# Optimization experiments

Hardware: AMD Instinct MI355X
Metric: run time of the kernel (lower is better)

## Reference

```python
import jax, jax.numpy as jnp
import numpy as np

HEADS = 8
DIM_HEAD = 64
LN_EPS = 1e-5


def _layernorm(x, gamma, beta):
    mu = jnp.mean(x, axis=-1, keepdims=True)
    var = jnp.var(x, axis=-1, keepdims=True)
    return (x - mu) * jax.lax.rsqrt(var + LN_EPS) * gamma + beta


def setup_inputs() -> dict:
    key = jax.random.key(0)
    ks = jax.random.split(key, 5)
    B, N, D = 1, 16384, 512
    return {
        "x": jax.random.normal(ks[0], (B, N, D), dtype=jnp.float32),
        "ln_gamma": jnp.ones((D,), dtype=jnp.float32),
        "ln_beta": jnp.zeros((D,), dtype=jnp.float32),
        "w_qkv": jax.random.normal(ks[1], (D, 3 * D), dtype=jnp.float32) * (D ** -0.5),
        "agent": jax.random.normal(ks[2], (HEADS, 512, DIM_HEAD), dtype=jnp.float32) * (DIM_HEAD ** -0.5),
        "w_out": jax.random.normal(ks[3], (D, D), dtype=jnp.float32) * (D ** -0.5),
        "b_out": jnp.zeros((D,), dtype=jnp.float32),
    }


def reference(x, ln_gamma, ln_beta, w_qkv, agent, w_out, b_out):
    # TransLayer: x + Mask_Agent_Attention(LayerNorm(x))
    B, N, D = x.shape
    xn = _layernorm(x, ln_gamma, ln_beta)

    qkv = xn @ w_qkv                                   # [B, N, 3D]
    q, k, v = jnp.split(qkv, 3, axis=-1)
    # [B, H, N, d]
    q = q.reshape(B, N, HEADS, DIM_HEAD).transpose(0, 2, 1, 3)
    k = k.reshape(B, N, HEADS, DIM_HEAD).transpose(0, 2, 1, 3)
    v = v.reshape(B, N, HEADS, DIM_HEAD).transpose(0, 2, 1, 3)

    scale = DIM_HEAD ** -0.5  # tem=0 -> classical 1/sqrt(d) scaling

    # agents aggregate values: softmax over keys  [B, H, A, N]
    attn1 = jax.nn.softmax(jnp.einsum('had,bhnd->bhan', agent, k) * scale, axis=-1)
    agent_v = jnp.einsum('bhan,bhnd->bhad', attn1, v)  # [B, H, A, d]

    # queries attend to agents: softmax over agents  [B, H, N, A]
    attn2 = jax.nn.softmax(jnp.einsum('bhnd,had->bhna', q, agent) * scale, axis=-1)
    out = jnp.einsum('bhna,bhad->bhnd', attn2, agent_v)  # [B, H, N, d]

    out = out + v  # residual=True: value residual inside attention
    out = out.transpose(0, 2, 1, 3).reshape(B, N, D)
    out = out @ w_out + b_out
    return x + out
```

## Files before the change

### kernel.cpp

```cpp
#include <hip/hip_runtime.h>
#include <stdint.h>

typedef unsigned short u16;
typedef __attribute__((ext_vector_type(8))) short bf16x8;
typedef __attribute__((ext_vector_type(4))) float f32x4;

__device__ __forceinline__ float bf2f(u16 u){
  union { uint32_t i; float f; } v; v.i = ((uint32_t)u) << 16; return v.f;
}
__device__ __forceinline__ u16 f2bf(float f){
  union { float fl; uint32_t i; } v; v.fl = f;
  uint32_t r = v.i + 0x7FFFu + ((v.i >> 16) & 1u);
  return (u16)(r >> 16);
}
__device__ __forceinline__ uint32_t cvt_pk_bf16(float lo, float hi){
  uint32_t r;
  asm("v_cvt_pk_bf16_f32 %0, %1, %2" : "=v"(r) : "v"(lo), "v"(hi));
  return r;
}
__device__ __forceinline__ f32x4 mfma16(bf16x8 a, bf16x8 b, f32x4 c){
  return __builtin_amdgcn_mfma_f32_16x16x32_bf16(a, b, c, 0, 0, 0);
}
__device__ __forceinline__ void gload16(const u16* g, u16* l){
  __builtin_amdgcn_global_load_lds((const __attribute__((address_space(1))) void*)g,
                                   (__attribute__((address_space(3))) void*)l, 16, 0, 0);
}

__global__ __launch_bounds__(256) void k_conv_bf(const float* __restrict__ in, u16* __restrict__ out, int n, float scale){
  int i = (blockIdx.x * 256 + threadIdx.x) * 4;
  if (i >= n) return;
  float4 v = *(const float4*)(in + i);
  ushort4 o; o.x=f2bf(v.x*scale); o.y=f2bf(v.y*scale); o.z=f2bf(v.z*scale); o.w=f2bf(v.w*scale);
  *(ushort4*)(out + i) = o;
}

__global__ __launch_bounds__(256) void k_transp(const float* __restrict__ in, u16* __restrict__ out, int R, int C){
  __shared__ u16 tile[64][68];
  int c0 = blockIdx.x * 64, r0 = blockIdx.y * 64;
  int tr = threadIdx.x >> 4;
  int tc = (threadIdx.x & 15) * 4;
  for (int rr = 0; rr < 4; rr++){
    int r = rr * 16 + tr;
    float4 v = *(const float4*)(in + (size_t)(r0 + r) * C + c0 + tc);
    ushort4 o; o.x=f2bf(v.x); o.y=f2bf(v.y); o.z=f2bf(v.z); o.w=f2bf(v.w);
    *(ushort4*)&tile[r][tc] = o;
  }
  __syncthreads();
  for (int rr = 0; rr < 4; rr++){
    int oc = rr * 16 + tr;
    ushort4 o;
    o.x = tile[tc+0][oc]; o.y = tile[tc+1][oc]; o.z = tile[tc+2][oc]; o.w = tile[tc+3][oc];
    *(ushort4*)(out + (size_t)(c0 + oc) * R + r0 + tc) = o;
  }
}

__global__ __launch_bounds__(256) void k_transp_v(const u16* __restrict__ qkv, u16* __restrict__ vT){
  __shared__ u16 tile[64][68];
  int n0 = blockIdx.x * 64;
  int c0 = blockIdx.y * 64;
  int tr = threadIdx.x >> 4;
  int tc = (threadIdx.x & 15) * 4;
  for (int rr = 0; rr < 4; rr++){
    int r = rr * 16 + tr;
    ushort4 v = *(const ushort4*)(qkv + (size_t)(n0 + r) * 1536 + 1024 + c0 + tc);
    *(ushort4*)&tile[r][tc] = v;
  }
  __syncthreads();
  for (int rr = 0; rr < 4; rr++){
    int oc = rr * 16 + tr;
    ushort4 o;
    o.x = tile[tc+0][oc]; o.y = tile[tc+1][oc]; o.z = tile[tc+2][oc]; o.w = tile[tc+3][oc];
    *(ushort4*)(vT + (size_t)(c0 + oc) * 16384 + n0 + tc) = o;
  }
}

__global__ __launch_bounds__(128) void k_ln(const float* __restrict__ x, const float* __restrict__ g,
                                            const float* __restrict__ b, u16* __restrict__ xn){
  int row = blockIdx.x;
  int t = threadIdx.x;
  float4 v = *(const float4*)(x + (size_t)row * 512 + t * 4);
  float s = v.x + v.y + v.z + v.w;
  float q = v.x*v.x + v.y*v.y + v.z*v.z + v.w*v.w;
  for (int o = 32; o > 0; o >>= 1){ s += __shfl_down(s, o); q += __shfl_down(q, o); }
  __shared__ float red[4];
  if ((t & 63) == 0){ red[(t >> 6) * 2] = s; red[(t >> 6) * 2 + 1] = q; }
  __syncthreads();
  float mu  = (red[0] + red[2]) * (1.0f/512.0f);
  float var = (red[1] + red[3]) * (1.0f/512.0f) - mu * mu;
  float rs = rsqrtf(var + 1e-5f);
  float4 gv = *(const float4*)(g + t * 4);
  float4 bv = *(const float4*)(b + t * 4);
  ushort4 o;
  o.x = f2bf((v.x - mu) * rs * gv.x + bv.x);
  o.y = f2bf((v.y - mu) * rs * gv.y + bv.y);
  o.z = f2bf((v.z - mu) * rs * gv.z + bv.z);
  o.w = f2bf((v.w - mu) * rs * gv.w + bv.w);
  *(ushort4*)(xn + (size_t)row * 512 + t * 4) = o;
}


__global__ __launch_bounds__(512) void k_gemm_qkv(const u16* __restrict__ A, const u16* __restrict__ Bt,
                                                  u16* __restrict__ C){
  __shared__ u16 aL[2][256 * 64];
  __shared__ u16 bL[2][128 * 64];
  int m0 = blockIdx.x * 256, n0 = blockIdx.y * 128;
  int t = threadIdx.x, w = t >> 6, l = t & 63;
  int wm = (w >> 1) * 64, wn = (w & 1) * 64;
  int lr = l & 15;
  int blkSrc = (l & 7) ^ ((l >> 3) & 7);
  const u16* gA = A  + (size_t)(m0 + w*8 + (l >> 3)) * 512 + blkSrc * 8;
  const u16* gB = Bt + (size_t)(n0 + w*8 + (l >> 3)) * 512 + blkSrc * 8;
  f32x4 acc[4][4];
  for (int i=0;i<4;i++) for (int j=0;j<4;j++) acc[i][j] = {0.f,0.f,0.f,0.f};

  auto stage = [&](int buf, int k0){
    #pragma unroll
    for (int p = 0; p < 4; p++)
      gload16(gA + (size_t)p*64*512 + k0, &aL[buf][(p*64 + w*8) * 64]);
    #pragma unroll
    for (int p = 0; p < 2; p++)
      gload16(gB + (size_t)p*64*512 + k0, &bL[buf][(p*64 + w*8) * 64]);
  };
  auto comp = [&](const u16* ab, const u16* bb){
    #pragma unroll
    for (int kk = 0; kk < 64; kk += 32){
      int xo = (((l >> 4) + (kk >> 3)) ^ (l & 7)) << 3;
      bf16x8 av[4], bv[4];
      #pragma unroll
      for (int mt=0;mt<4;mt++) av[mt] = *(const bf16x8*)&ab[(wm + mt*16 + lr)*64 + xo];
      #pragma unroll
      for (int nt=0;nt<4;nt++) bv[nt] = *(const bf16x8*)&bb[(wn + nt*16 + lr)*64 + xo];
      #pragma unroll
      for (int mt=0;mt<4;mt++)
        #pragma unroll
        for (int nt=0;nt<4;nt++)
          acc[mt][nt] = mfma16(av[mt], bv[nt], acc[mt][nt]);
    }
  };

  stage(0, 0);
  __syncthreads();
  #pragma unroll
  for (int tk = 0; tk < 8; tk++){
    int cur = tk & 1;
    if (tk < 7) stage(cur ^ 1, (tk + 1) * 64);
    comp(&aL[cur][0], &bL[cur][0]);
    __syncthreads();
  }

  int rr = (l >> 4) * 4, cc = l & 15;
  for (int mt=0;mt<4;mt++) for (int nt=0;nt<4;nt++)
    for (int j=0;j<4;j++){
      int r = m0 + wm + mt*16 + rr + j;
      int c = n0 + wn + nt*16 + cc;
      C[(size_t)r * 1536 + c] = f2bf(acc[mt][nt][j]);
    }
}

__global__ __launch_bounds__(512) void k_gemm_out(const u16* __restrict__ A, const u16* __restrict__ Bt,
                                                  const float* __restrict__ x, const float* __restrict__ bias,
                                                  float* __restrict__ y){
  __shared__ u16 aL[2][256 * 64];
  __shared__ u16 bL[2][128 * 64];
  int m0 = blockIdx.x * 256, n0 = blockIdx.y * 128;
  int t = threadIdx.x, w = t >> 6, l = t & 63;
  int wm = (w >> 1) * 64, wn = (w & 1) * 64;
  int lr = l & 15;
  int blkSrc = (l & 7) ^ ((l >> 3) & 7);
  const u16* gA = A  + (size_t)(m0 + w*8 + (l >> 3)) * 512 + blkSrc * 8;
  const u16* gB = Bt + (size_t)(n0 + w*8 + (l >> 3)) * 512 + blkSrc * 8;
  f32x4 acc[4][4];
  for (int i=0;i<4;i++) for (int j=0;j<4;j++) acc[i][j] = {0.f,0.f,0.f,0.f};

  auto stage = [&](int buf, int k0){
    #pragma unroll
    for (int p = 0; p < 4; p++)
      gload16(gA + (size_t)p*64*512 + k0, &aL[buf][(p*64 + w*8) * 64]);
    #pragma unroll
    for (int p = 0; p < 2; p++)
      gload16(gB + (size_t)p*64*512 + k0, &bL[buf][(p*64 + w*8) * 64]);
  };
  auto comp = [&](const u16* ab, const u16* bb){
    #pragma unroll
    for (int kk = 0; kk < 64; kk += 32){
      int xo = (((l >> 4) + (kk >> 3)) ^ (l & 7)) << 3;
      bf16x8 av[4], bv[4];
      #pragma unroll
      for (int mt=0;mt<4;mt++) av[mt] = *(const bf16x8*)&ab[(wm + mt*16 + lr)*64 + xo];
      #pragma unroll
      for (int nt=0;nt<4;nt++) bv[nt] = *(const bf16x8*)&bb[(wn + nt*16 + lr)*64 + xo];
      #pragma unroll
      for (int mt=0;mt<4;mt++)
        #pragma unroll
        for (int nt=0;nt<4;nt++)
          acc[mt][nt] = mfma16(av[mt], bv[nt], acc[mt][nt]);
    }
  };

  stage(0, 0);
  __syncthreads();
  #pragma unroll
  for (int tk = 0; tk < 8; tk++){
    int cur = tk & 1;
    if (tk < 7) stage(cur ^ 1, (tk + 1) * 64);
    comp(&aL[cur][0], &bL[cur][0]);
    __syncthreads();
  }

  int rr = (l >> 4) * 4, cc = l & 15;
  for (int mt=0;mt<4;mt++) for (int nt=0;nt<4;nt++)
    for (int j=0;j<4;j++){
      int r = m0 + wm + mt*16 + rr + j;
      int c = n0 + wn + nt*16 + cc;
      y[(size_t)r * 512 + c] = acc[mt][nt][j] + bias[c] + x[(size_t)r * 512 + c];
    }
}

__global__ __launch_bounds__(256) void k_agent_agg(const u16* __restrict__ agbf, const u16* __restrict__ qkv,
                                                   const u16* __restrict__ vT,
                                                   float* __restrict__ nump, float* __restrict__ denp){
  int L = blockIdx.x;
  int g = (L >> 6) * 8 + (L & 7);
  int m = (L >> 3) & 7;
  int h = g >> 4, ch = g & 15, a0 = m * 64;

  __shared__ u16 ag[64][72];
  __shared__ u16 kt[64][72];
  __shared__ u16 vt[64][72];
  __shared__ u16 pt[64][72];
  int t = threadIdx.x, w = t >> 6, l = t & 63;

  for (int i = 0; i < 2; i++){
    int flat = t + 256 * i;
    int r = flat >> 3, c = (flat & 7) * 8;
    *(uint4*)&ag[r][c] = *(const uint4*)(agbf + (size_t)(h * 512 + a0 + r) * 64 + c);
  }

  bf16x8 ones;
  for (int i = 0; i < 8; i++) ones[i] = (short)0x3F80;

  f32x4 acc2[4];
  for (int i=0;i<4;i++) acc2[i] = {0.f,0.f,0.f,0.f};
  f32x4 accd = {0.f,0.f,0.f,0.f};

  for (int sub = 0; sub < 16; sub++){
    int n0 = ch * 1024 + sub * 64;
    __syncthreads();
    {
      int flat = t;
      int r = flat >> 3, c = (flat & 7) * 8;
      *(uint4*)&kt[r][c] = *(const uint4*)(qkv + (size_t)(n0 + r) * 1536 + 512 + h * 64 + c);
      int flat2 = t + 256;
      int r2 = flat2 >> 3, c2 = (flat2 & 7) * 8;
      *(uint4*)&kt[r2][c2] = *(const uint4*)(qkv + (size_t)(n0 + r2) * 1536 + 512 + h * 64 + c2);
      *(uint4*)&vt[r][c]   = *(const uint4*)(vT + ((size_t)(h * 64 + r) << 14) + n0 + c);
      *(uint4*)&vt[r2][c2] = *(const uint4*)(vT + ((size_t)(h * 64 + r2) << 14) + n0 + c2);
    }
    __syncthreads();

    f32x4 s[4];
    for (int nt=0;nt<4;nt++) s[nt] = {0.f,0.f,0.f,0.f};
    for (int kk = 0; kk < 64; kk += 32){
      int kb = kk + (l >> 4) * 8;
      bf16x8 kf = *(const bf16x8*)&kt[w*16 + (l & 15)][kb];
      for (int nt=0;nt<4;nt++){
        bf16x8 af = *(const bf16x8*)&ag[nt*16 + (l & 15)][kb];
        s[nt] = mfma16(kf, af, s[nt]);
      }
    }
    int nb = w*16 + (l >> 4) * 4;
    for (int nt=0;nt<4;nt++){
      int a = nt*16 + (l & 15);
      uint32_t w0 = cvt_pk_bf16(__builtin_amdgcn_exp2f(s[nt][0]), __builtin_amdgcn_exp2f(s[nt][1]));
      uint32_t w1 = cvt_pk_bf16(__builtin_amdgcn_exp2f(s[nt][2]), __builtin_amdgcn_exp2f(s[nt][3]));
      uint2 o; o.x = w0; o.y = w1;
      *(uint2*)&pt[a][nb] = o;
    }
    __syncthreads();

    for (int kk = 0; kk < 64; kk += 32){
      int kb = kk + (l >> 4) * 8;
      bf16x8 vf = *(const bf16x8*)&vt[w*16 + (l & 15)][kb];
      for (int mt=0;mt<4;mt++){
        bf16x8 pf = *(const bf16x8*)&pt[mt*16 + (l & 15)][kb];
        acc2[mt] = mfma16(pf, vf, acc2[mt]);
      }
      bf16x8 pw = *(const bf16x8*)&pt[w*16 + (l & 15)][kb];
      accd = mfma16(ones, pw, accd);
    }
  }

  size_t base = ((size_t)(h * 16 + ch) * 512 + a0) * 64;
  for (int mt=0;mt<4;mt++)
    #pragma unroll
    for (int j=0;j<4;j++){
      int a = mt*16 + (l>>4)*4 + j;
      int d = w*16 + (l&15);
      nump[base + (size_t)a*64 + d] = acc2[mt][j];
    }
  if (l < 16) denp[(size_t)(h*16 + ch) * 512 + a0 + w*16 + l] = accd[0];
}

__global__ __launch_bounds__(64) void k_agent_reduce(const float* __restrict__ nump, const float* __restrict__ denp,
                                                     u16* __restrict__ avtg){
  int h = blockIdx.x >> 9;
  int a = blockIdx.x & 511;
  int d = threadIdx.x;
  float num = 0.f, den = 0.f;
  for (int c = 0; c < 16; c++){
    num += nump[((size_t)(h * 16 + c) * 512 + a) * 64 + d];
    den += denp[(size_t)(h * 16 + c) * 512 + a];
  }
  avtg[((size_t)h * 64 + d) * 512 + a] = f2bf(num / den);
}

__global__ __launch_bounds__(256) void k_qattn(const u16* __restrict__ qkv, const u16* __restrict__ agbf,
                                               const u16* __restrict__ avtg, u16* __restrict__ atto){
  int n0 = blockIdx.x * 64;
  int h  = blockIdx.y;
  __shared__ u16 qt[64][72];
  __shared__ u16 ag[64][72];
  __shared__ u16 avt[64][72];
  __shared__ u16 pt[64][72];
  __shared__ float dnf[64];
  int t = threadIdx.x, w = t >> 6, l = t & 63;

  for (int i = 0; i < 2; i++){
    int flat = t + 256 * i;
    int r = flat >> 3, c = (flat & 7) * 8;
    *(uint4*)&qt[r][c] = *(const uint4*)(qkv + (size_t)(n0 + r) * 1536 + h * 64 + c);
  }

  bf16x8 ones;
  for (int i = 0; i < 8; i++) ones[i] = (short)0x3F80;

  f32x4 acc[4];
  for (int i=0;i<4;i++) acc[i] = {0.f,0.f,0.f,0.f};
  f32x4 accd = {0.f,0.f,0.f,0.f};

  for (int at = 0; at < 8; at++){
    int a0 = at * 64;
    __syncthreads();
    for (int i = 0; i < 2; i++){
      int flat = t + 256 * i;
      int r = flat >> 3, c = (flat & 7) * 8;
      *(uint4*)&ag[r][c]  = *(const uint4*)(agbf + (size_t)(h * 512 + a0 + r) * 64 + c);
      *(uint4*)&avt[r][c] = *(const uint4*)(avtg + (size_t)(h * 64 + r) * 512 + a0 + c);
    }
    __syncthreads();

    f32x4 s[4];
    for (int nt=0;nt<4;nt++) s[nt] = {0.f,0.f,0.f,0.f};
    for (int kk = 0; kk < 64; kk += 32){
      int kb = kk + (l >> 4) * 8;
      bf16x8 af = *(const bf16x8*)&ag[w*16 + (l & 15)][kb];
      for (int nt=0;nt<4;nt++){
        bf16x8 qf = *(const bf16x8*)&qt[nt*16 + (l & 15)][kb];
        s[nt] = mfma16(af, qf, s[nt]);
      }
    }
    int ab = w*16 + (l >> 4) * 4;
    for (int nt=0;nt<4;nt++){
      int n = nt*16 + (l & 15);
      uint32_t w0 = cvt_pk_bf16(__builtin_amdgcn_exp2f(s[nt][0]), __builtin_amdgcn_exp2f(s[nt][1]));
      uint32_t w1 = cvt_pk_bf16(__builtin_amdgcn_exp2f(s[nt][2]), __builtin_amdgcn_exp2f(s[nt][3]));
      uint2 o; o.x = w0; o.y = w1;
      *(uint2*)&pt[n][ab] = o;
    }
    __syncthreads();

    for (int kk = 0; kk < 64; kk += 32){
      int kb = kk + (l >> 4) * 8;
      bf16x8 vf = *(const bf16x8*)&avt[w*16 + (l & 15)][kb];
      for (int mt=0;mt<4;mt++){
        bf16x8 pf = *(const bf16x8*)&pt[mt*16 + (l & 15)][kb];
        acc[mt] = mfma16(pf, vf, acc[mt]);
      }
      bf16x8 pw = *(const bf16x8*)&pt[w*16 + (l & 15)][kb];
      accd = mfma16(ones, pw, accd);
    }
  }

  if (l < 16) dnf[w*16 + l] = accd[0];
  __syncthreads();
  if (t < 64) dnf[t] = __builtin_amdgcn_rcpf(dnf[t]);
  __syncthreads();

  int d = w*16 + (l & 15);
  for (int mt=0;mt<4;mt++){
    #pragma unroll
    for (int j=0;j<4;j++){
      int n = mt*16 + (l>>4)*4 + j;
      float v = bf2f(qkv[(size_t)(n0 + n) * 1536 + 1024 + h * 64 + d]);
      atto[(size_t)(n0 + n) * 512 + h * 64 + d] = f2bf(acc[mt][j] * dnf[n] + v);
    }
  }
}

extern "C" void kernel_launch(void* const* d_in, const int* in_sizes, int n_in,
                              void* d_out, int out_size, void* d_ws, size_t ws_size,
                              hipStream_t stream) {
  const float* x     = (const float*)d_in[0];
  const float* gamma = (const float*)d_in[1];
  const float* beta  = (const float*)d_in[2];
  const float* w_qkv = (const float*)d_in[3];
  const float* agent = (const float*)d_in[4];
  const float* w_out = (const float*)d_in[5];
  const float* b_out = (const float*)d_in[6];
  float* y = (float*)d_out;

  char* ws = (char*)d_ws;
  u16*   xn    = (u16*)  (ws + 0);
  u16*   vT    = (u16*)  (ws + 0);
  u16*   qkv   = (u16*)  (ws + 16777216);
  u16*   wqkvt = (u16*)  (ws + 67108864);
  u16*   woutt = (u16*)  (ws + 68681728);
  u16*   agbf  = (u16*)  (ws + 69206016);
  u16*   avtg  = (u16*)  (ws + 69730304);
  u16*   atto  = (u16*)  (ws + 70254592);
  float* nump  = (float*)(ws + 87031808);
  float* denp  = (float*)(ws + 103809024);

  k_conv_bf   <<<dim3(256),     dim3(256), 0, stream>>>(agent, agbf, 8*512*64, 0.125f * 1.44269504089f);
  k_transp    <<<dim3(24, 8),   dim3(256), 0, stream>>>(w_qkv, wqkvt, 512, 1536);
  k_transp    <<<dim3(8, 8),    dim3(256), 0, stream>>>(w_out, woutt, 512, 512);
  k_ln        <<<dim3(16384),   dim3(128), 0, stream>>>(x, gamma, beta, xn);
  k_gemm_qkv  <<<dim3(64, 12),  dim3(512), 0, stream>>>(xn, wqkvt, qkv);
  k_transp_v  <<<dim3(256, 8),  dim3(256), 0, stream>>>(qkv, vT);
  k_agent_agg <<<dim3(1024),    dim3(256), 0, stream>>>(agbf, qkv, vT, nump, denp);
  k_agent_reduce<<<dim3(4096),  dim3(64),  0, stream>>>(nump, denp, avtg);
  k_qattn     <<<dim3(256, 8),  dim3(256), 0, stream>>>(qkv, agbf, avtg, atto);
  k_gemm_out  <<<dim3(64, 4),   dim3(512), 0, stream>>>(atto, woutt, x, b_out, y);
}
```

Baseline: 167.6 us.

## Restructure query-attention kernel with register P, agent-split warps and register prefetch

The query-to-agent attention kernel now keeps Q fragments and the exp-score tile in registers and feeds P straight into the second MFMA, with no LDS round trip for P. Each warp handles a different slice of agents for all 64 rows and d columns, processes 128 agents per step, and prefetches the next agent/agent-V tile into registers. The per-warp partial outputs and denominators are reduced across warps through LDS at the end, and the residual add and bf16 store are vectorized. This removes per-tile syncs and P shared-memory traffic, at the cost of more accumulator registers (64 floats) and an LDS cross-warp reduction.

```diff
diff --git a/kernel.cpp b/kernel.cpp
--- a/kernel.cpp
+++ b/kernel.cpp
@@ -318,81 +318,156 @@
                                                const u16* __restrict__ avtg, u16* __restrict__ atto){
   int n0 = blockIdx.x * 64;
   int h  = blockIdx.y;
-  __shared__ u16 qt[64][72];
-  __shared__ u16 ag[64][72];
-  __shared__ u16 avt[64][72];
-  __shared__ u16 pt[64][72];
-  __shared__ float dnf[64];
+  __shared__ char sm[35840];
+  __shared__ float dnf[4][64];
+  u16 (*agL)[72]  = (u16(*)[72])sm;
+  u16 (*avL)[136] = (u16(*)[136])(sm + 18432);
+  float* red0 = (float*)sm;
+  float* red1 = red0 + 64*68;
+
   int t = threadIdx.x, w = t >> 6, l = t & 63;
-
-  for (int i = 0; i < 2; i++){
-    int flat = t + 256 * i;
-    int r = flat >> 3, c = (flat & 7) * 8;
-    *(uint4*)&qt[r][c] = *(const uint4*)(qkv + (size_t)(n0 + r) * 1536 + h * 64 + c);
-  }
-
-  bf16x8 ones;
-  for (int i = 0; i < 8; i++) ones[i] = (short)0x3F80;
-
-  f32x4 acc[4];
-  for (int i=0;i<4;i++) acc[i] = {0.f,0.f,0.f,0.f};
-  f32x4 accd = {0.f,0.f,0.f,0.f};
-
-  for (int at = 0; at < 8; at++){
-    int a0 = at * 64;
-    __syncthreads();
-    for (int i = 0; i < 2; i++){
-      int flat = t + 256 * i;
-      int r = flat >> 3, c = (flat & 7) * 8;
-      *(uint4*)&ag[r][c]  = *(const uint4*)(agbf + (size_t)(h * 512 + a0 + r) * 64 + c);
-      *(uint4*)&avt[r][c] = *(const uint4*)(avtg + (size_t)(h * 64 + r) * 512 + a0 + c);
-    }
-    __syncthreads();
-
-    f32x4 s[4];
-    for (int nt=0;nt<4;nt++) s[nt] = {0.f,0.f,0.f,0.f};
-    for (int kk = 0; kk < 64; kk += 32){
-      int kb = kk + (l >> 4) * 8;
-      bf16x8 af = *(const bf16x8*)&ag[w*16 + (l & 15)][kb];
+  int lr = l & 15, q4 = l >> 4;
+
+  bf16x8 qf[4][2];
+  #pragma unroll
+  for (int nt=0;nt<4;nt++)
+    #pragma unroll
+    for (int kk=0;kk<2;kk++)
+      qf[nt][kk] = *(const bf16x8*)(qkv + (size_t)(n0 + nt*16 + lr) * 1536 + h*64 + kk*32 + q4*8);
+
+  uint4 sAg[4], sAv[4];
+  #pragma unroll
+  for (int i=0;i<4;i++){
+    int c = t + 256*i;
+    sAg[i] = *(const uint4*)(agbf + (size_t)(h*512 + (c>>3)) * 64 + (c&7)*8);
+    sAv[i] = *(const uint4*)(avtg + (size_t)(h*64 + (c>>4)) * 512 + (c&15)*8);
+  }
+
+  f32x4 acc[4][4];
+  #pragma unroll
+  for (int i=0;i<4;i++)
+    #pragma unroll
+    for (int j=0;j<4;j++) acc[i][j] = {0.f,0.f,0.f,0.f};
+  float den[4] = {0.f,0.f,0.f,0.f};
+
+  for (int p = 0; p < 4; p++){
+    __syncthreads();
+    #pragma unroll
+    for (int i=0;i<4;i++){
+      int c = t + 256*i;
+      *(uint4*)&agL[c>>3][(c&7)*8]  = sAg[i];
+      *(uint4*)&avL[c>>4][(c&15)*8] = sAv[i];
+    }
+    __syncthreads();
+    if (p < 3){
+      #pragma unroll
+      for (int i=0;i<4;i++){
+        int c = t + 256*i;
+        sAg[i] = *(const uint4*)(agbf + (size_t)(h*512 + (p+1)*128 + (c>>3)) * 64 + (c&7)*8);
+        sAv[i] = *(const uint4*)(avtg + (size_t)(h*64 + (c>>4)) * 512 + (p+1)*128 + (c&15)*8);
+      }
+    }
+
+    uint32_t pk[2][4][2];
+    #pragma unroll
+    for (int t2 = 0; t2 < 2; t2++){
+      f32x4 s[4];
+      #pragma unroll
+      for (int nt=0;nt<4;nt++) s[nt] = {0.f,0.f,0.f,0.f};
+      #pragma unroll
+      for (int kk=0;kk<2;kk++){
+        bf16x8 af = *(const bf16x8*)&agL[t2*64 + w*16 + lr][q4*8 + kk*32];
+        #pragma unroll
+        for (int nt=0;nt<4;nt++)
+          s[nt] = mfma16(af, qf[nt][kk], s[nt]);
+      }
+      #pragma unroll
       for (int nt=0;nt<4;nt++){
-        bf16x8 qf = *(const bf16x8*)&qt[nt*16 + (l & 15)][kb];
-        s[nt] = mfma16(af, qf, s[nt]);
+        float e0 = __builtin_amdgcn_exp2f(s[nt][0]);
+        float e1 = __builtin_amdgcn_exp2f(s[nt][1]);
+        float e2 = __builtin_amdgcn_exp2f(s[nt][2]);
+        float e3 = __builtin_amdgcn_exp2f(s[nt][3]);
+        den[nt] += (e0 + e1) + (e2 + e3);
+        pk[t2][nt][0] = cvt_pk_bf16(e0, e1);
+        pk[t2][nt][1] = cvt_pk_bf16(e2, e3);
       }
     }
-    int ab = w*16 + (l >> 4) * 4;
-    for (int nt=0;nt<4;nt++){
-      int n = nt*16 + (l & 15);
-      uint32_t w0 = cvt_pk_bf16(__builtin_amdgcn_exp2f(s[nt][0]), __builtin_amdgcn_exp2f(s[nt][1]));
-      uint32_t w1 = cvt_pk_bf16(__builtin_amdgcn_exp2f(s[nt][2]), __builtin_amdgcn_exp2f(s[nt][3]));
-      uint2 o; o.x = w0; o.y = w1;
-      *(uint2*)&pt[n][ab] = o;
-    }
-    __syncthreads();
-
-    for (int kk = 0; kk < 64; kk += 32){
-      int kb = kk + (l >> 4) * 8;
-      bf16x8 vf = *(const bf16x8*)&avt[w*16 + (l & 15)][kb];
-      for (int mt=0;mt<4;mt++){
-        bf16x8 pf = *(const bf16x8*)&pt[mt*16 + (l & 15)][kb];
-        acc[mt] = mfma16(pf, vf, acc[mt]);
+    #pragma unroll
+    for (int dt=0;dt<4;dt++){
+      uint2 b0 = *(const uint2*)&avL[dt*16 + lr][w*16 + q4*4];
+      uint2 b1 = *(const uint2*)&avL[dt*16 + lr][64 + w*16 + q4*4];
+      union { uint32_t u[4]; bf16x8 v; } bb;
+      bb.u[0] = b0.x; bb.u[1] = b0.y; bb.u[2] = b1.x; bb.u[3] = b1.y;
+      #pragma unroll
+      for (int nt=0;nt<4;nt++){
+        union { uint32_t u[4]; bf16x8 v; } aa;
+        aa.u[0] = pk[0][nt][0]; aa.u[1] = pk[0][nt][1];
+        aa.u[2] = pk[1][nt][0]; aa.u[3] = pk[1][nt][1];
+        acc[nt][dt] = mfma16(aa.v, bb.v, acc[nt][dt]);
       }
-      bf16x8 pw = *(const bf16x8*)&pt[w*16 + (l & 15)][kb];
-      accd = mfma16(ones, pw, accd);
-    }
-  }
-
-  if (l < 16) dnf[w*16 + l] = accd[0];
-  __syncthreads();
-  if (t < 64) dnf[t] = __builtin_amdgcn_rcpf(dnf[t]);
-  __syncthreads();
-
-  int d = w*16 + (l & 15);
-  for (int mt=0;mt<4;mt++){
-    #pragma unroll
-    for (int j=0;j<4;j++){
-      int n = mt*16 + (l>>4)*4 + j;
-      float v = bf2f(qkv[(size_t)(n0 + n) * 1536 + 1024 + h * 64 + d]);
-      atto[(size_t)(n0 + n) * 512 + h * 64 + d] = f2bf(acc[mt][j] * dnf[n] + v);
+    }
+  }
+
+  float dq[4];
+  #pragma unroll
+  for (int nt=0;nt<4;nt++){
+    float r = den[nt];
+    r += __shfl_xor(r, 16);
+    r += __shfl_xor(r, 32);
+    dq[nt] = r;
+  }
+  __syncthreads();
+  if (q4 == 0)
+    #pragma unroll
+    for (int nt=0;nt<4;nt++) dnf[w][nt*16 + lr] = dq[nt];
+  if (w < 2){
+    float* r = (w == 0) ? red0 : red1;
+    #pragma unroll
+    for (int nt=0;nt<4;nt++)
+      #pragma unroll
+      for (int dt=0;dt<4;dt++)
+        #pragma unroll
+        for (int j=0;j<4;j++)
+          r[(nt*16 + q4*4 + j)*68 + dt*16 + lr] = acc[nt][dt][j];
+  }
+  __syncthreads();
+  if (w >= 2){
+    float* r = (w == 2) ? red0 : red1;
+    #pragma unroll
+    for (int nt=0;nt<4;nt++)
+      #pragma unroll
+      for (int dt=0;dt<4;dt++)
+        #pragma unroll
+        for (int j=0;j<4;j++)
+          r[(nt*16 + q4*4 + j)*68 + dt*16 + lr] += acc[nt][dt][j];
+  }
+  __syncthreads();
+
+  {
+    int n = t & 63, db = t >> 6;
+    float dsum = dnf[0][n] + dnf[1][n] + dnf[2][n] + dnf[3][n];
+    float rc = __builtin_amdgcn_rcpf(dsum);
+    const u16* vres = qkv + (size_t)(n0 + n) * 1536 + 1024 + h*64 + db*16;
+    u16* op = atto + (size_t)(n0 + n) * 512 + h*64 + db*16;
+    #pragma unroll
+    for (int half = 0; half < 2; half++){
+      f32x4 ra = *(f32x4*)&red0[n*68 + db*16 + half*8];
+      f32x4 rb = *(f32x4*)&red0[n*68 + db*16 + half*8 + 4];
+      f32x4 sa = *(f32x4*)&red1[n*68 + db*16 + half*8];
+      f32x4 sb = *(f32x4*)&red1[n*68 + db*16 + half*8 + 4];
+      ushort4 v0 = *(const ushort4*)(vres + half*8);
+      ushort4 v1 = *(const ushort4*)(vres + half*8 + 4);
+      ushort4 o0, o1;
+      o0.x = f2bf((ra[0]+sa[0])*rc + bf2f(v0.x));
+      o0.y = f2bf((ra[1]+sa[1])*rc + bf2f(v0.y));
+      o0.z = f2bf((ra[2]+sa[2])*rc + bf2f(v0.z));
+      o0.w = f2bf((ra[3]+sa[3])*rc + bf2f(v0.w));
+      o1.x = f2bf((rb[0]+sb[0])*rc + bf2f(v1.x));
+      o1.y = f2bf((rb[1]+sb[1])*rc + bf2f(v1.y));
+      o1.z = f2bf((rb[2]+sb[2])*rc + bf2f(v1.z));
+      o1.w = f2bf((rb[3]+sb[3])*rc + bf2f(v1.w));
+      *(ushort4*)(op + half*8) = o0;
+      *(ushort4*)(op + half*8 + 4) = o1;
     }
   }
 }
```

Result: slower. 211.9 us (+26.4%).
